# Optimization experiments

Hardware: AMD Instinct MI355X
Metric: run time of the kernel (lower is better)

Reference implementation:

```python
import jax, jax.numpy as jnp
import numpy as np

NUM_HEADS = 32
HEAD_DIM = 128
NUM_KV_HEADS = 8
SCALE = 0.08838834764831845  # 1/sqrt(128)
SEQ_LEN = 2048


def setup_inputs() -> dict:
    key = jax.random.key(0)
    kq, kk, kv = jax.random.split(key, 3)
    q = jax.random.normal(kq, (SEQ_LEN, NUM_HEADS * HEAD_DIM), dtype=jnp.float32)
    k = jax.random.normal(kk, (SEQ_LEN, NUM_KV_HEADS * HEAD_DIM), dtype=jnp.float32)
    v = jax.random.normal(kv, (SEQ_LEN, NUM_KV_HEADS * HEAD_DIM), dtype=jnp.float32)
    return {"q": q, "k": k, "v": v}


def reference(q, k, v):
    S = q.shape[0]
    qh = q.reshape(S, NUM_HEADS, HEAD_DIM)            # [S, H, D]
    kh = k.reshape(S, NUM_KV_HEADS, HEAD_DIM)         # [S, KVH, D]
    vh = v.reshape(S, NUM_KV_HEADS, HEAD_DIM)
    # GQA: repeat_interleave along head dim
    expand = NUM_HEADS // NUM_KV_HEADS
    kh = jnp.repeat(kh, expand, axis=1)               # [S, H, D]
    vh = jnp.repeat(vh, expand, axis=1)
    scores = jnp.einsum('ihd,jhd->ihj', qh, kh) * SCALE  # [S, H, S]
    causal = jnp.triu(jnp.ones((S, S), dtype=bool), k=1)  # True above diagonal
    scores = jnp.where(causal[:, None, :], jnp.float32(-jnp.inf), scores)
    weights = jax.nn.softmax(scores, axis=-1)
    o = jnp.einsum('ihj,jhd->ihd', weights, vh)       # [S, H, D]
    return o.reshape(S, NUM_HEADS * HEAD_DIM)
```

## Files before the change

### kernel.cpp

```cpp
#include <hip/hip_runtime.h>


#define SEQ   2048
#define NH    32
#define NKV   8
#define HD    128
#define QLD   4096
#define KLD   1024
#define KVB   32

typedef __attribute__((ext_vector_type(8))) __bf16 bf16x8;
typedef __attribute__((ext_vector_type(4))) __bf16 bf16x4;
typedef __attribute__((ext_vector_type(2))) __bf16 bf16x2;
typedef __attribute__((ext_vector_type(4))) float  f32x4;
typedef __attribute__((ext_vector_type(4))) short  s16x4;
typedef __attribute__((ext_vector_type(2))) unsigned int u32x2;

static __device__ __forceinline__ unsigned int pack2(float lo, float hi) {
  bf16x2 t; t[0] = (__bf16)lo; t[1] = (__bf16)hi;
  return __builtin_bit_cast(unsigned int, t);
}

static __device__ __forceinline__ f32x4 mfma16(bf16x4 a, u32x2 b, f32x4 c) {
#if __has_builtin(__builtin_amdgcn_mfma_f32_16x16x16bf16_1k)
  return __builtin_amdgcn_mfma_f32_16x16x16bf16_1k(
      __builtin_bit_cast(s16x4, a), __builtin_bit_cast(s16x4, b), c, 0, 0, 0);
#else
  asm volatile("v_mfma_f32_16x16x16_bf16 %0, %1, %2, %0"
               : "+v"(c) : "v"(a), "v"(b));
  return c;
#endif
}

__global__ void prep_tiles(const float* __restrict__ k, __bf16* __restrict__ kt,
                           const float* __restrict__ v, __bf16* __restrict__ vtt) {
  __shared__ __bf16 TT[HD][34];
  const int bx  = blockIdx.x;
  const int tid = threadIdx.x;
  const int kl  = tid >> 3;
  const int dc  = tid & 7;
  if (bx < 512) {
    const int kvh = bx >> 6, t = bx & 63;
    const float* src = k + (size_t)(t * 32 + kl) * KLD + kvh * HD + dc * 16;
    __bf16* dst = kt + (size_t)(kvh * 64 + t) * 4096;
    const int g = kl >> 4, l15 = kl & 15;
#pragma unroll
    for (int h = 0; h < 2; ++h) {
      const int d0 = dc * 16 + h * 8;
      const int c = d0 >> 5, quad = (d0 >> 3) & 3;
      float4 a0 = *(const float4*)(src + h * 8);
      float4 a1 = *(const float4*)(src + h * 8 + 4);
      bf16x8 f;
      f[0] = (__bf16)a0.x; f[1] = (__bf16)a0.y; f[2] = (__bf16)a0.z; f[3] = (__bf16)a0.w;
      f[4] = (__bf16)a1.x; f[5] = (__bf16)a1.y; f[6] = (__bf16)a1.z; f[7] = (__bf16)a1.w;
      const int slot = g * 256 + c * 64 + quad * 16 + l15;
      *(bf16x8*)(dst + slot * 8) = f;
    }
  } else {
    const int b = bx - 512, kvh = b >> 6, t = b & 63;
    const float* src = v + (size_t)(t * 32 + kl) * KLD + kvh * HD + dc * 16;
#pragma unroll
    for (int jj = 0; jj < 4; ++jj) {
      float4 x = *(const float4*)(src + jj * 4);
      const int d = dc * 16 + jj * 4;
      TT[d + 0][kl] = (__bf16)x.x; TT[d + 1][kl] = (__bf16)x.y;
      TT[d + 2][kl] = (__bf16)x.z; TT[d + 3][kl] = (__bf16)x.w;
    }
    __syncthreads();
    __bf16* dst = vtt + (size_t)(kvh * 64 + t) * 4096;
#pragma unroll
    for (int ss = 0; ss < 2; ++ss) {
      const int s   = tid + ss * 256;
      const int nt  = s >> 6, quad = (s >> 4) & 3, l15 = s & 15;
      const int dim = nt * 16 + l15;
      bf16x8 f;
#pragma unroll
      for (int e = 0; e < 4; ++e) {
        f[e]     = TT[dim][quad * 4 + e];
        f[4 + e] = TT[dim][16 + quad * 4 + e];
      }
      *(bf16x8*)(dst + s * 8) = f;
    }
  }
}

__global__ __launch_bounds__(512, 4)
void fa_kernel(const float* __restrict__ q, const __bf16* __restrict__ kt,
               const __bf16* __restrict__ vtt, float* __restrict__ out) {
  __shared__ float CAcc[4][2048];
  __shared__ float CLp[4][256];

  const int bid  = blockIdx.x;
  const int kvh  = bid & 7;
  const int slot = bid >> 3;
  const int head = kvh * 4 + (slot & 3);
  const int ip   = slot >> 2;
  const int tid  = threadIdx.x;
  const int w    = tid >> 6;
  const int wg   = w >> 2;
  const int wl   = w & 3;
  const int lane = tid & 63;
  const int l15  = lane & 15;
  const int quad = lane >> 4;

  constexpr float QS = 0.08838834764831845f * 1.4426950408889634f;

  const __bf16* KT0 = kt  + (size_t)(kvh * 64) * 4096;
  const __bf16* VT0 = vtt + (size_t)(kvh * 64) * 4096;
  const int loff = lane * 8;

  auto phase = [&](int rowtile, int t0, int nkt) {
    const int rowbase = rowtile * 64 + wl * 16;

    bf16x8 qf[4];
    {
      const float* qp = q + (size_t)(rowbase + l15) * QLD + head * HD + quad * 8;
#pragma unroll
      for (int c = 0; c < 4; ++c) {
        float4 a0 = *(const float4*)(qp + c * 32);
        float4 a1 = *(const float4*)(qp + c * 32 + 4);
        bf16x8 f;
        f[0] = (__bf16)(a0.x * QS); f[1] = (__bf16)(a0.y * QS);
        f[2] = (__bf16)(a0.z * QS); f[3] = (__bf16)(a0.w * QS);
        f[4] = (__bf16)(a1.x * QS); f[5] = (__bf16)(a1.y * QS);
        f[6] = (__bf16)(a1.z * QS); f[7] = (__bf16)(a1.w * QS);
        qf[c] = f;
      }
    }

    f32x4 acc[8];
    f32x4 lp = (f32x4){0.f, 0.f, 0.f, 0.f};
#pragma unroll
    for (int nt = 0; nt < 8; ++nt) acc[nt] = (f32x4){0.f, 0.f, 0.f, 0.f};

    for (int tt = 0; tt < nkt; ++tt) {
      const int t = t0 + tt;

      bf16x8 kk[2][4];
      {
        const __bf16* ktile = KT0 + (size_t)t * 4096;
#pragma unroll
        for (int g = 0; g < 2; ++g)
#pragma unroll
          for (int c = 0; c < 4; ++c)
            kk[g][c] = *(const bf16x8*)(ktile + g * 2048 + c * 512 + loff);
      }

      u32x2 pknew[2];
#pragma unroll
      for (int g = 0; g < 2; ++g) {
        f32x4 s = (f32x4){0.f, 0.f, 0.f, 0.f};
        __builtin_amdgcn_s_setprio(1);
#pragma unroll
        for (int c = 0; c < 4; ++c)
          s = __builtin_amdgcn_mfma_f32_16x16x32_bf16(kk[g][c], qf[c], s, 0, 0, 0);
        __builtin_amdgcn_s_setprio(0);
        if (t * KVB + KVB - 1 > rowbase) {
          const int key0  = t * KVB + g * 16 + quad * 4;
          const int myrow = rowbase + l15;
#pragma unroll
          for (int e = 0; e < 4; ++e)
            if (key0 + e > myrow) s[e] = -1e30f;
        }
        f32x4 p;
#pragma unroll
        for (int e = 0; e < 4; ++e) p[e] = __builtin_amdgcn_exp2f(s[e]);
        lp += p;
        u32x2 pkk;
        pkk.x = pack2(p[0], p[1]);
        pkk.y = pack2(p[2], p[3]);
        pknew[g] = pkk;
      }

      bf16x8 vv[8];
      {
        const __bf16* vtile = VT0 + (size_t)t * 4096;
#pragma unroll
        for (int nt = 0; nt < 8; ++nt)
          vv[nt] = *(const bf16x8*)(vtile + nt * 512 + loff);
      }

#pragma unroll
      for (int kt2 = 0; kt2 < 2; ++kt2) {
        __builtin_amdgcn_s_setprio(1);
#pragma unroll
        for (int nt = 0; nt < 8; ++nt) {
          bf16x4 vf;
#pragma unroll
          for (int e = 0; e < 4; ++e) vf[e] = vv[nt][kt2 * 4 + e];
          acc[nt] = mfma16(vf, pknew[kt2], acc[nt]);
        }
        __builtin_amdgcn_s_setprio(0);
      }
      __builtin_amdgcn_s_barrier();
    }

    if (wg == 1) {
#pragma unroll
      for (int nt = 0; nt < 8; ++nt)
        *(f32x4*)&CAcc[wl][nt * 256 + lane * 4] = acc[nt];
      *(f32x4*)&CLp[wl][lane * 4] = lp;
    }
    __syncthreads();
    if (wg == 0) {
      f32x4 plp = *(const f32x4*)&CLp[wl][lane * 4];
      lp += plp;
      float ls = lp[0] + lp[1] + lp[2] + lp[3];
      ls += __shfl_xor(ls, 16);
      ls += __shfl_xor(ls, 32);
      const float inv = 1.0f / ls;
      float* op = out + (size_t)(rowbase + l15) * QLD + head * HD + quad * 4;
#pragma unroll
      for (int nt = 0; nt < 8; ++nt) {
        f32x4 pa = *(const f32x4*)&CAcc[wl][nt * 256 + lane * 4];
        f32x4 r = acc[nt] + pa;
        float4 wv = {r[0] * inv, r[1] * inv, r[2] * inv, r[3] * inv};
        *(float4*)(op + nt * 16) = wv;
      }
    }
    __syncthreads();
  };

  const int nH = 32 - ip;
  phase(31 - ip, wg * nH, nH);
  const int nL = ip + 1;
  phase(ip, wg * nL, nL);
}

extern "C" void kernel_launch(void* const* d_in, const int* in_sizes, int n_in,
                              void* d_out, int out_size, void* d_ws, size_t ws_size,
                              hipStream_t stream) {
  const float* q = (const float*)d_in[0];
  const float* k = (const float*)d_in[1];
  const float* v = (const float*)d_in[2];
  float* o = (float*)d_out;
  __bf16* ktb = (__bf16*)d_ws;
  __bf16* vtb = (__bf16*)d_ws + (size_t)SEQ * KLD;
  prep_tiles<<<1024, 256, 0, stream>>>(k, ktb, v, vtb);
  fa_kernel<<<512, 512, 0, stream>>>(q, ktb, vtb, o);
}
```

Before: 168.0 us.

## Give each wave two query sub-tiles to reuse loaded K/V fragments

Each wave now handles 32 query rows (two 16-row sub-tiles) instead of 16, so every K and V fragment loaded from global memory feeds twice as many MFMAs. The block shrinks from 8 to 4 waves, and the per-iteration s_barrier inside the key loop is removed. The aim is to halve redundant K/V load traffic per query row and cut synchronisation. In exchange, register pressure per wave roughly doubles for accumulators and Q fragments, and there are fewer waves per block to hide latency.

```diff
diff --git a/kernel.cpp b/kernel.cpp
--- a/kernel.cpp
+++ b/kernel.cpp
@@ -84,11 +84,11 @@
   }
 }
 
-__global__ __launch_bounds__(512, 4)
+__global__ __launch_bounds__(256, 2)
 void fa_kernel(const float* __restrict__ q, const __bf16* __restrict__ kt,
                const __bf16* __restrict__ vtt, float* __restrict__ out) {
-  __shared__ float CAcc[4][2048];
-  __shared__ float CLp[4][256];
+  __shared__ float CAcc[2][2][8][256];
+  __shared__ float CLp[2][2][256];
 
   const int bid  = blockIdx.x;
   const int kvh  = bid & 7;
@@ -97,8 +97,8 @@
   const int ip   = slot >> 2;
   const int tid  = threadIdx.x;
   const int w    = tid >> 6;
-  const int wg   = w >> 2;
-  const int wl   = w & 3;
+  const int rw   = w & 1;
+  const int wg   = w >> 1;
   const int lane = tid & 63;
   const int l15  = lane & 15;
   const int quad = lane >> 4;
@@ -110,11 +110,12 @@
   const int loff = lane * 8;
 
   auto phase = [&](int rowtile, int t0, int nkt) {
-    const int rowbase = rowtile * 64 + wl * 16;
-
-    bf16x8 qf[4];
-    {
-      const float* qp = q + (size_t)(rowbase + l15) * QLD + head * HD + quad * 8;
+    const int rowbase = rowtile * 64 + rw * 32;
+
+    bf16x8 qf[2][4];
+#pragma unroll
+    for (int sub = 0; sub < 2; ++sub) {
+      const float* qp = q + (size_t)(rowbase + sub * 16 + l15) * QLD + head * HD + quad * 8;
 #pragma unroll
       for (int c = 0; c < 4; ++c) {
         float4 a0 = *(const float4*)(qp + c * 32);
@@ -124,14 +125,18 @@
         f[2] = (__bf16)(a0.z * QS); f[3] = (__bf16)(a0.w * QS);
         f[4] = (__bf16)(a1.x * QS); f[5] = (__bf16)(a1.y * QS);
         f[6] = (__bf16)(a1.z * QS); f[7] = (__bf16)(a1.w * QS);
-        qf[c] = f;
-      }
-    }
-
-    f32x4 acc[8];
-    f32x4 lp = (f32x4){0.f, 0.f, 0.f, 0.f};
-#pragma unroll
-    for (int nt = 0; nt < 8; ++nt) acc[nt] = (f32x4){0.f, 0.f, 0.f, 0.f};
+        qf[sub][c] = f;
+      }
+    }
+
+    f32x4 acc[2][8];
+    f32x4 lp[2];
+#pragma unroll
+    for (int sub = 0; sub < 2; ++sub) {
+      lp[sub] = (f32x4){0.f, 0.f, 0.f, 0.f};
+#pragma unroll
+      for (int nt = 0; nt < 8; ++nt) acc[sub][nt] = (f32x4){0.f, 0.f, 0.f, 0.f};
+    }
 
     for (int tt = 0; tt < nkt; ++tt) {
       const int t = t0 + tt;
@@ -145,33 +150,6 @@
           for (int c = 0; c < 4; ++c)
             kk[g][c] = *(const bf16x8*)(ktile + g * 2048 + c * 512 + loff);
       }
-
-      u32x2 pknew[2];
-#pragma unroll
-      for (int g = 0; g < 2; ++g) {
-        f32x4 s = (f32x4){0.f, 0.f, 0.f, 0.f};
-        __builtin_amdgcn_s_setprio(1);
-#pragma unroll
-        for (int c = 0; c < 4; ++c)
-          s = __builtin_amdgcn_mfma_f32_16x16x32_bf16(kk[g][c], qf[c], s, 0, 0, 0);
-        __builtin_amdgcn_s_setprio(0);
-        if (t * KVB + KVB - 1 > rowbase) {
-          const int key0  = t * KVB + g * 16 + quad * 4;
-          const int myrow = rowbase + l15;
-#pragma unroll
-          for (int e = 0; e < 4; ++e)
-            if (key0 + e > myrow) s[e] = -1e30f;
-        }
-        f32x4 p;
-#pragma unroll
-        for (int e = 0; e < 4; ++e) p[e] = __builtin_amdgcn_exp2f(s[e]);
-        lp += p;
-        u32x2 pkk;
-        pkk.x = pack2(p[0], p[1]);
-        pkk.y = pack2(p[2], p[3]);
-        pknew[g] = pkk;
-      }
-
       bf16x8 vv[8];
       {
         const __bf16* vtile = VT0 + (size_t)t * 4096;
@@ -180,6 +158,36 @@
           vv[nt] = *(const bf16x8*)(vtile + nt * 512 + loff);
       }
 
+      u32x2 pk[2][2];
+#pragma unroll
+      for (int g = 0; g < 2; ++g) {
+#pragma unroll
+        for (int sub = 0; sub < 2; ++sub) {
+          f32x4 s = (f32x4){0.f, 0.f, 0.f, 0.f};
+          __builtin_amdgcn_s_setprio(1);
+#pragma unroll
+          for (int c = 0; c < 4; ++c)
+            s = __builtin_amdgcn_mfma_f32_16x16x32_bf16(kk[g][c], qf[sub][c], s, 0, 0, 0);
+          __builtin_amdgcn_s_setprio(0);
+          const int rb = rowbase + sub * 16;
+          if (t * KVB + KVB - 1 > rb) {
+            const int key0  = t * KVB + g * 16 + quad * 4;
+            const int myrow = rb + l15;
+#pragma unroll
+            for (int e = 0; e < 4; ++e)
+              if (key0 + e > myrow) s[e] = -1e30f;
+          }
+          f32x4 p;
+#pragma unroll
+          for (int e = 0; e < 4; ++e) p[e] = __builtin_amdgcn_exp2f(s[e]);
+          lp[sub] += p;
+          u32x2 pkk;
+          pkk.x = pack2(p[0], p[1]);
+          pkk.y = pack2(p[2], p[3]);
+          pk[sub][g] = pkk;
+        }
+      }
+
 #pragma unroll
       for (int kt2 = 0; kt2 < 2; ++kt2) {
         __builtin_amdgcn_s_setprio(1);
@@ -188,34 +196,41 @@
           bf16x4 vf;
 #pragma unroll
           for (int e = 0; e < 4; ++e) vf[e] = vv[nt][kt2 * 4 + e];
-          acc[nt] = mfma16(vf, pknew[kt2], acc[nt]);
+          acc[0][nt] = mfma16(vf, pk[0][kt2], acc[0][nt]);
+          acc[1][nt] = mfma16(vf, pk[1][kt2], acc[1][nt]);
         }
         __builtin_amdgcn_s_setprio(0);
       }
-      __builtin_amdgcn_s_barrier();
-    }
-
+    }
+
+    __syncthreads();
     if (wg == 1) {
 #pragma unroll
-      for (int nt = 0; nt < 8; ++nt)
-        *(f32x4*)&CAcc[wl][nt * 256 + lane * 4] = acc[nt];
-      *(f32x4*)&CLp[wl][lane * 4] = lp;
+      for (int sub = 0; sub < 2; ++sub) {
+#pragma unroll
+        for (int nt = 0; nt < 8; ++nt)
+          *(f32x4*)&CAcc[rw][sub][nt][lane * 4] = acc[sub][nt];
+        *(f32x4*)&CLp[rw][sub][lane * 4] = lp[sub];
+      }
     }
     __syncthreads();
     if (wg == 0) {
-      f32x4 plp = *(const f32x4*)&CLp[wl][lane * 4];
-      lp += plp;
-      float ls = lp[0] + lp[1] + lp[2] + lp[3];
-      ls += __shfl_xor(ls, 16);
-      ls += __shfl_xor(ls, 32);
-      const float inv = 1.0f / ls;
-      float* op = out + (size_t)(rowbase + l15) * QLD + head * HD + quad * 4;
-#pragma unroll
-      for (int nt = 0; nt < 8; ++nt) {
-        f32x4 pa = *(const f32x4*)&CAcc[wl][nt * 256 + lane * 4];
-        f32x4 r = acc[nt] + pa;
-        float4 wv = {r[0] * inv, r[1] * inv, r[2] * inv, r[3] * inv};
-        *(float4*)(op + nt * 16) = wv;
+#pragma unroll
+      for (int sub = 0; sub < 2; ++sub) {
+        f32x4 plp = *(const f32x4*)&CLp[rw][sub][lane * 4];
+        f32x4 l = lp[sub] + plp;
+        float ls = l[0] + l[1] + l[2] + l[3];
+        ls += __shfl_xor(ls, 16);
+        ls += __shfl_xor(ls, 32);
+        const float inv = 1.0f / ls;
+        float* op = out + (size_t)(rowbase + sub * 16 + l15) * QLD + head * HD + quad * 4;
+#pragma unroll
+        for (int nt = 0; nt < 8; ++nt) {
+          f32x4 pa = *(const f32x4*)&CAcc[rw][sub][nt][lane * 4];
+          f32x4 r = acc[sub][nt] + pa;
+          float4 wv = {r[0] * inv, r[1] * inv, r[2] * inv, r[3] * inv};
+          *(float4*)(op + nt * 16) = wv;
+        }
       }
     }
     __syncthreads();
@@ -237,5 +252,5 @@
   __bf16* ktb = (__bf16*)d_ws;
   __bf16* vtb = (__bf16*)d_ws + (size_t)SEQ * KLD;
   prep_tiles<<<1024, 256, 0, stream>>>(k, ktb, v, vtb);
-  fa_kernel<<<512, 512, 0, stream>>>(q, ktb, vtb, o);
-}
+  fa_kernel<<<512, 256, 0, stream>>>(q, ktb, vtb, o);
+}
```

Result: faster. 136.3 us (-18.9%).
